# Kernel optimization log

Hardware: AMD Instinct MI355X
Metric: run time of the kernel (lower is better)

Reference implementation:

```python
import jax, jax.numpy as jnp
import numpy as np

N_PATCHES = 14
HIDDEN_D = 768
N_HEADS = 12
D_HEAD = HIDDEN_D // N_HEADS
OUT_D = 1000
IMG = 224
C = 3
PS = IMG // N_PATCHES  # 16
SEQ = N_PATCHES * N_PATCHES + 1  # 197
INPUT_D = C * PS * PS  # 768
EPS = 1e-5


def positional_embeddings(s, d):
    i = jnp.arange(s, dtype=jnp.float32)[:, None]
    j = jnp.arange(d, dtype=jnp.float32)[None, :]
    even = jnp.sin(i / jnp.power(10000.0, j / d))
    odd = jnp.cos(i / jnp.power(10000.0, (j - 1.0) / d))
    return jnp.where(jnp.arange(d)[None, :] % 2 == 0, even, odd)


def layernorm_2d(x, g, b):
    # torch nn.LayerNorm((S, D)): normalize over last two dims jointly, biased var
    mu = jnp.mean(x, axis=(-2, -1), keepdims=True)
    var = jnp.var(x, axis=(-2, -1), keepdims=True)
    return (x - mu) * jax.lax.rsqrt(var + EPS) * g + b


def setup_inputs() -> dict:
    key = jax.random.key(0)
    ks = jax.random.split(key, 16)
    s = 0.02
    return {
        "images": jax.random.normal(ks[0], (64, C, IMG, IMG), jnp.float32),
        "W_map": jax.random.normal(ks[1], (INPUT_D, HIDDEN_D), jnp.float32) * s,
        "b_map": jnp.zeros((HIDDEN_D,), jnp.float32),
        "cls_tok": jax.random.uniform(ks[2], (1, HIDDEN_D), jnp.float32),
        "ln1_g": jnp.ones((SEQ, HIDDEN_D), jnp.float32),
        "ln1_b": jnp.zeros((SEQ, HIDDEN_D), jnp.float32),
        "Wq": jax.random.normal(ks[3], (N_HEADS, D_HEAD, D_HEAD), jnp.float32) * s,
        "bq": jnp.zeros((N_HEADS, D_HEAD), jnp.float32),
        "Wk": jax.random.normal(ks[4], (N_HEADS, D_HEAD, D_HEAD), jnp.float32) * s,
        "bk": jnp.zeros((N_HEADS, D_HEAD), jnp.float32),
        "Wv": jax.random.normal(ks[5], (N_HEADS, D_HEAD, D_HEAD), jnp.float32) * s,
        "bv": jnp.zeros((N_HEADS, D_HEAD), jnp.float32),
        "ln2_g": jnp.ones((SEQ, HIDDEN_D), jnp.float32),
        "ln2_b": jnp.zeros((SEQ, HIDDEN_D), jnp.float32),
        "W_enc": jax.random.normal(ks[6], (HIDDEN_D, HIDDEN_D), jnp.float32) * s,
        "b_enc": jnp.zeros((HIDDEN_D,), jnp.float32),
        "W_out": jax.random.normal(ks[7], (HIDDEN_D, OUT_D), jnp.float32) * s,
        "b_out": jnp.zeros((OUT_D,), jnp.float32),
    }


def reference(images, W_map, b_map, cls_tok, ln1_g, ln1_b, Wq, bq, Wk, bk, Wv, bv,
              ln2_g, ln2_b, W_enc, b_enc, W_out, b_out):
    n = images.shape[0]
    # patchify: [N,C,H,W] -> [N, np*np, C*ps*ps], patch flattened in (C,ph,pw) order
    p = images.reshape(n, C, N_PATCHES, PS, N_PATCHES, PS)
    patches = p.transpose(0, 2, 4, 1, 3, 5).reshape(n, N_PATCHES * N_PATCHES, INPUT_D)

    tokens = patches @ W_map + b_map  # [N, np^2, D]
    cls = jnp.broadcast_to(cls_tok[None], (n, 1, HIDDEN_D))
    tokens = jnp.concatenate([cls, tokens], axis=1)  # [N, S, D]
    tokens = tokens + positional_embeddings(SEQ, HIDDEN_D)[None]

    # MSA on ln1(tokens), vectorized over batch and heads
    x = layernorm_2d(tokens, ln1_g, ln1_b)
    xh = x.reshape(n, SEQ, N_HEADS, D_HEAD)  # split hidden into heads
    q = jnp.einsum('bshd,hde->bshe', xh, Wq) + bq[None, None]
    k = jnp.einsum('bshd,hde->bshe', xh, Wk) + bk[None, None]
    v = jnp.einsum('bshd,hde->bshe', xh, Wv) + bv[None, None]
    scores = jnp.einsum('bshe,bthe->bhst', q, k) / np.sqrt(D_HEAD).astype(np.float32)
    attn = jax.nn.softmax(scores, axis=-1)  # [B,H,S,S]
    msa = jnp.einsum('bhst,bthe->bshe', attn, v).reshape(n, SEQ, HIDDEN_D)

    out = tokens + msa
    out = out + jax.nn.relu(layernorm_2d(out, ln2_g, ln2_b) @ W_enc + b_enc)
    cls_out = out[:, 0]  # [N, D]
    return jax.nn.softmax(cls_out @ W_out + b_out, axis=-1)
```

## Files before the change

kernel.cpp:

```cpp
#include <hip/hip_runtime.h>
#include <math.h>

#define SEQL 197
#define HD 768
#define NH 12
#define DHD 64
#define BATCH 64
#define OUTD 1000

typedef unsigned short ushort_t;
typedef __attribute__((ext_vector_type(8))) short bf16x8;
typedef __attribute__((ext_vector_type(4))) float f32x4;

static __device__ __forceinline__ unsigned short f2bf(float f) {
    union { float f; unsigned u; } v; v.f = f;
    unsigned r = v.u + 0x7fff + ((v.u >> 16) & 1);
    return (unsigned short)(r >> 16);
}

static __device__ __forceinline__ void gload16(const ushort_t* g, ushort_t* l) {
    __builtin_amdgcn_global_load_lds(
        (const __attribute__((address_space(1))) unsigned int*)g,
        (__attribute__((address_space(3))) unsigned int*)l, 16, 0, 0);
}

__global__ void k_init(const float* __restrict__ cls_tok, float* __restrict__ pos,
                       float* __restrict__ tok, float* __restrict__ stats) {
    int i = blockIdx.x * 256 + threadIdx.x;
    if (i < SEQL * HD) {
        int s = i / HD, d = i % HD;
        float f = (float)(d & ~1);
        float r = powf(10000.0f, -f / (float)HD);
        float a = (float)s * r;
        pos[i] = (d & 1) ? cosf(a) : sinf(a);
    } else {
        int j = i - SEQL * HD;
        if (j < BATCH * HD) {
            int b = j / HD, e = j % HD;
            float v = cls_tok[e] + ((e & 1) ? 1.0f : 0.0f);
            tok[(b * SEQL) * HD + e] = v;
            float sv = v, qv = v * v;
#pragma unroll
            for (int off = 32; off > 0; off >>= 1) {
                sv += __shfl_down(sv, off);
                qv += __shfl_down(qv, off);
            }
            if ((threadIdx.x & 63) == 0) {
                atomicAdd(&stats[2 * b], sv);
                atomicAdd(&stats[2 * b + 1], qv);
            }
        }
    }
}

__global__ void k_cvtAll(const float* __restrict__ W_map, const float* __restrict__ W_enc,
                         const float* __restrict__ Wq, const float* __restrict__ Wk,
                         const float* __restrict__ Wv,
                         ushort_t* __restrict__ WmT, ushort_t* __restrict__ WeT,
                         ushort_t* __restrict__ wt, float* __restrict__ stats) {
    int idx = blockIdx.x * 256 + threadIdx.x;
    if (blockIdx.x == 0 && threadIdx.x < 256) stats[threadIdx.x] = 0.f;
    if (idx < 2 * 147456) {
        const float* W = (idx < 147456) ? W_map : W_enc;
        ushort_t* WT   = (idx < 147456) ? WmT : WeT;
        int i = (idx < 147456) ? idx : idx - 147456;
        int k = i / 192, nq = i % 192;
        float4 w = *(const float4*)&W[k * 768 + nq * 4];
        WT[(nq * 4 + 0) * 768 + k] = f2bf(w.x);
        WT[(nq * 4 + 1) * 768 + k] = f2bf(w.y);
        WT[(nq * 4 + 2) * 768 + k] = f2bf(w.z);
        WT[(nq * 4 + 3) * 768 + k] = f2bf(w.w);
    } else {
        int i = idx - 2 * 147456;
        if (i < 36864) {
            int dq = i & 15;
            int e  = (i >> 4) & 63;
            int h  = (i >> 10) % 12;
            int pj = i / 12288;
            const float* W = (pj == 0) ? Wq : (pj == 1) ? Wk : Wv;
            ushort4 o;
            o.x = f2bf(W[(h * 64 + dq * 4 + 0) * 64 + e]);
            o.y = f2bf(W[(h * 64 + dq * 4 + 1) * 64 + e]);
            o.z = f2bf(W[(h * 64 + dq * 4 + 2) * 64 + e]);
            o.w = f2bf(W[(h * 64 + dq * 4 + 3) * 64 + e]);
            *(ushort4*)&wt[(size_t)((pj * 12 + h) * 64 + e) * 64 + dq * 4] = o;
        }
    }
}

__global__ void k_prep_patches(const float* __restrict__ img, ushort_t* __restrict__ Ae) {
    int idx = blockIdx.x * 256 + threadIdx.x;
    int m = idx / 192, kq = idx % 192;
    int k0 = kq * 4;
    int c = k0 >> 8, rem = k0 & 255, ir = rem >> 4, jc = rem & 15;
    int b = m / 196, pi = m % 196;
    int pr = pi / 14, pc = pi % 14;
    float4 v = *(const float4*)&img[((b * 3 + c) * 224 + pr * 16 + ir) * 224 + pc * 16 + jc];
    ushort4 o;
    o.x = f2bf(v.x); o.y = f2bf(v.y); o.z = f2bf(v.z); o.w = f2bf(v.w);
    *(ushort4*)&Ae[m * 768 + k0] = o;
}

template <int MODE>
__launch_bounds__(256)
__global__ void k_gemm_bf16(const ushort_t* __restrict__ A, const ushort_t* __restrict__ Bt,
                            const float* __restrict__ bias, const float* __restrict__ pos,
                            float* __restrict__ out, int Mtot, float* __restrict__ stats) {
    __shared__ ushort_t As[128 * 64];
    __shared__ ushort_t Bs[128 * 64];
    __shared__ float redS[4][4];
    const int m0 = blockIdx.x * 128;
    const int n0 = blockIdx.y * 128;
    const int tid = threadIdx.x;
    const int lane = tid & 63, wave = tid >> 6;
    const int wm = wave >> 1, wn = wave & 1;

    f32x4 acc[4][4];
#pragma unroll
    for (int i = 0; i < 4; ++i)
#pragma unroll
        for (int j = 0; j < 4; ++j)
#pragma unroll
            for (int r = 0; r < 4; ++r) acc[i][j][r] = 0.f;

    for (int kt = 0; kt < 12; ++kt) {
        const int k0 = kt * 64;
#pragma unroll
        for (int t = 0; t < 4; ++t) {
            int c = (wave << 2) | t;
            int o = c * 1024 + lane * 16;
            int row = o >> 7;
            int inner = o & 127;
            int col = (inner ^ ((row & 7) << 4)) >> 1;
            gload16(&A[(size_t)(m0 + row) * 768 + k0 + col], &As[c * 512]);
            gload16(&Bt[(size_t)(n0 + row) * 768 + k0 + col], &Bs[c * 512]);
        }
        __syncthreads();
#pragma unroll
        for (int ks = 0; ks < 2; ++ks) {
            const int cbyte = ks * 64 + (lane >> 4) * 16;
            bf16x8 af[4], bf[4];
#pragma unroll
            for (int mi = 0; mi < 4; ++mi) {
                int row = wm * 64 + mi * 16 + (lane & 15);
                af[mi] = *(const bf16x8*)((const char*)As + row * 128 + (cbyte ^ ((row & 7) << 4)));
            }
#pragma unroll
            for (int ni = 0; ni < 4; ++ni) {
                int n = wn * 64 + ni * 16 + (lane & 15);
                bf[ni] = *(const bf16x8*)((const char*)Bs + n * 128 + (cbyte ^ ((n & 7) << 4)));
            }
#pragma unroll
            for (int mi = 0; mi < 4; ++mi)
#pragma unroll
                for (int ni = 0; ni < 4; ++ni)
                    acc[mi][ni] = __builtin_amdgcn_mfma_f32_16x16x32_bf16(af[mi], bf[ni], acc[mi][ni], 0, 0, 0);
        }
        __syncthreads();
    }

    const int colb = n0 + wn * 64 + (lane & 15);
    const int rowb = m0 + wm * 64 + (lane >> 4) * 4;
    float s_lo = 0.f, q_lo = 0.f, s_hi = 0.f, q_hi = 0.f;
    const int bA = m0 / 196;
    const int mSplit = (bA + 1) * 196;
#pragma unroll
    for (int ni = 0; ni < 4; ++ni) {
        const int n = colb + ni * 16;
        const float bn = bias[n];
#pragma unroll
        for (int mi = 0; mi < 4; ++mi) {
#pragma unroll
            for (int r = 0; r < 4; ++r) {
                int m = rowb + mi * 16 + r;
                if (MODE == 0) {
                    int b = m / 196, s = 1 + m % 196;
                    float oval = acc[mi][ni][r] + bn + pos[s * HD + n];
                    out[((b * SEQL) + s) * HD + n] = oval;
                    if (m < mSplit) { s_lo += oval; q_lo += oval * oval; }
                    else            { s_hi += oval; q_hi += oval * oval; }
                } else {
                    if (m < Mtot) {
                        float* p = &out[(size_t)m * HD + n];
                        *p = *p + fmaxf(acc[mi][ni][r] + bn, 0.f);
                    }
                }
            }
        }
    }
    if (MODE == 0) {
#pragma unroll
        for (int off = 32; off > 0; off >>= 1) {
            s_lo += __shfl_down(s_lo, off);
            q_lo += __shfl_down(q_lo, off);
            s_hi += __shfl_down(s_hi, off);
            q_hi += __shfl_down(q_hi, off);
        }
        if (lane == 0) {
            redS[wave][0] = s_lo; redS[wave][1] = q_lo;
            redS[wave][2] = s_hi; redS[wave][3] = q_hi;
        }
        __syncthreads();
        if (tid == 0) {
            float a0 = 0.f, a1 = 0.f, a2 = 0.f, a3 = 0.f;
#pragma unroll
            for (int i = 0; i < 4; ++i) {
                a0 += redS[i][0]; a1 += redS[i][1];
                a2 += redS[i][2]; a3 += redS[i][3];
            }
            atomicAdd(&stats[2 * bA], a0);
            atomicAdd(&stats[2 * bA + 1], a1);
            int bB = bA + 1;
            if (bB < BATCH) {
                atomicAdd(&stats[2 * bB], a2);
                atomicAdd(&stats[2 * bB + 1], a3);
            }
        }
    }
}

__launch_bounds__(512, 2)
__global__ void k_qkvattn(const float* __restrict__ tok, float* __restrict__ stats,
                          const float* __restrict__ g1, const float* __restrict__ b1,
                          const ushort_t* __restrict__ wt,
                          const float* __restrict__ bq, const float* __restrict__ bk,
                          const float* __restrict__ bv, float* __restrict__ out) {
    const int h = blockIdx.x, b = blockIdx.y;
    __shared__ __attribute__((aligned(16))) ushort_t sm[51712];
    __shared__ float rS[8], rS2[8];
    const int tid = threadIdx.x;
    const int wave = tid >> 6, lane = tid & 63;
    const int l16 = lane & 15, l4 = lane >> 4;
    const int r0 = wave * 32;
    const float inv_n = 1.0f / (float)(SEQL * HD);
    const float S1_ = stats[b * 2], S2_ = stats[b * 2 + 1];
    const float mu = S1_ * inv_n;
    const float rsg = rsqrtf(S2_ * inv_n - mu * mu + 1e-5f);

    {
        const int row = tid >> 1, hw = tid & 1;
        if (row < SEQL) {
            const float* tp = &tok[((size_t)b * SEQL + row) * HD + h * 64 + hw * 32];
            const float* gp = &g1[(size_t)row * HD + h * 64 + hw * 32];
            const float* bp = &b1[(size_t)row * HD + h * 64 + hw * 32];
#pragma unroll
            for (int g = 0; g < 4; ++g) {
                float4 t0 = *(const float4*)&tp[g * 8];
                float4 t1 = *(const float4*)&tp[g * 8 + 4];
                float4 ga = *(const float4*)&gp[g * 8];
                float4 gb = *(const float4*)&gp[g * 8 + 4];
                float4 ba = *(const float4*)&bp[g * 8];
                float4 bb = *(const float4*)&bp[g * 8 + 4];
                bf16x8 o;
                o[0] = (short)f2bf((t0.x - mu) * rsg * ga.x + ba.x);
                o[1] = (short)f2bf((t0.y - mu) * rsg * ga.y + ba.y);
                o[2] = (short)f2bf((t0.z - mu) * rsg * ga.z + ba.z);
                o[3] = (short)f2bf((t0.w - mu) * rsg * ga.w + ba.w);
                o[4] = (short)f2bf((t1.x - mu) * rsg * gb.x + bb.x);
                o[5] = (short)f2bf((t1.y - mu) * rsg * gb.y + bb.y);
                o[6] = (short)f2bf((t1.z - mu) * rsg * gb.z + bb.z);
                o[7] = (short)f2bf((t1.w - mu) * rsg * gb.w + bb.w);
                int pc = (hw * 32 + g * 8) ^ ((row & 7) << 3);
                *(bf16x8*)&sm[row * 64 + pc] = o;
            }
        } else {
            bf16x8 z;
#pragma unroll
            for (int j = 0; j < 8; ++j) z[j] = 0;
#pragma unroll
            for (int g = 0; g < 4; ++g) {
                int pc = (hw * 32 + g * 8) ^ ((row & 7) << 3);
                *(bf16x8*)&sm[row * 64 + pc] = z;
            }
        }
    }

    bf16x8 af[2][2];
#pragma unroll
    for (int mi = 0; mi < 2; ++mi)
#pragma unroll
        for (int kk = 0; kk < 2; ++kk) {
            int row = r0 + mi * 16 + l16;
            af[mi][kk] = *(const bf16x8*)&sm[row * 64 + ((kk * 32 + l4 * 8) ^ ((row & 7) << 3))];
        }

    ushort_t* myS = &sm[wave * 2048];

#define PROJ_ACC(PJ, ACC)                                                                      \
    {                                                                                          \
        _Pragma("unroll") for (int ni = 0; ni < 4; ++ni) {                                     \
            const ushort_t* wr = &wt[(size_t)(((PJ) * 12 + h) * 64 + ni * 16 + l16) * 64];     \
            bf16x8 w0 = *(const bf16x8*)&wr[l4 * 8];                                           \
            bf16x8 w1 = *(const bf16x8*)&wr[32 + l4 * 8];                                      \
            _Pragma("unroll") for (int mi = 0; mi < 2; ++mi) {                                 \
                ACC[mi][ni] = __builtin_amdgcn_mfma_f32_16x16x32_bf16(af[mi][0], w0, ACC[mi][ni], 0, 0, 0); \
                ACC[mi][ni] = __builtin_amdgcn_mfma_f32_16x16x32_bf16(af[mi][1], w1, ACC[mi][ni], 0, 0, 0); \
            }                                                                                  \
        }                                                                                      \
    }

    f32x4 acc[2][4];
#define ZERO_ACC                                                                               \
    _Pragma("unroll") for (int mi = 0; mi < 2; ++mi)                                           \
        _Pragma("unroll") for (int ni = 0; ni < 4; ++ni) {                                     \
            acc[mi][ni][0] = 0.f; acc[mi][ni][1] = 0.f; acc[mi][ni][2] = 0.f; acc[mi][ni][3] = 0.f; }

    ZERO_ACC;
    PROJ_ACC(0, acc);
#pragma unroll
    for (int ni = 0; ni < 4; ++ni) {
        float bn = bq[h * 64 + ni * 16 + l16];
#pragma unroll
        for (int mi = 0; mi < 2; ++mi)
#pragma unroll
            for (int r = 0; r < 4; ++r) {
                int rl = mi * 16 + l4 * 4 + r;
                myS[rl * 64 + ((ni * 16 + l16) ^ ((rl & 7) << 3))] = f2bf(acc[mi][ni][r] + bn);
            }
    }
    bf16x8 qa[2][2];
#pragma unroll
    for (int mi = 0; mi < 2; ++mi)
#pragma unroll
        for (int kk = 0; kk < 2; ++kk) {
            int rl = mi * 16 + l16;
            qa[mi][kk] = *(const bf16x8*)&myS[rl * 64 + ((kk * 32 + l4 * 8) ^ ((rl & 7) << 3))];
        }

    ZERO_ACC;
    PROJ_ACC(1, acc);
#pragma unroll
    for (int ni = 0; ni < 4; ++ni) {
        float bn = bk[h * 64 + ni * 16 + l16];
#pragma unroll
        for (int mi = 0; mi < 2; ++mi)
#pragma unroll
            for (int r = 0; r < 4; ++r) {
                int t = r0 + mi * 16 + l4 * 4 + r;
                sm[16384 + t * 72 + ni * 16 + l16] = f2bf(acc[mi][ni][r] + bn);
            }
    }

    ZERO_ACC;
    PROJ_ACC(2, acc);
#pragma unroll
    for (int ni = 0; ni < 4; ++ni) {
        float bn = bv[h * 64 + ni * 16 + l16];
#pragma unroll
        for (int mi = 0; mi < 2; ++mi)
#pragma unroll
            for (int r = 0; r < 4; ++r) {
                int t = r0 + mi * 16 + l4 * 4 + r;
                sm[34816 + (ni * 16 + l16) * 264 + t] = f2bf(acc[mi][ni][r] + bn);
            }
    }

    __syncthreads();

    f32x4 sa[2][16];
#pragma unroll
    for (int ni = 0; ni < 16; ++ni) {
        int t = ni * 16 + l16;
        bf16x8 k0 = *(const bf16x8*)&sm[16384 + t * 72 + l4 * 8];
        bf16x8 k1 = *(const bf16x8*)&sm[16384 + t * 72 + 32 + l4 * 8];
#pragma unroll
        for (int mi = 0; mi < 2; ++mi) {
            f32x4 z;
            z[0] = 0.f; z[1] = 0.f; z[2] = 0.f; z[3] = 0.f;
            z = __builtin_amdgcn_mfma_f32_16x16x32_bf16(qa[mi][0], k0, z, 0, 0, 0);
            sa[mi][ni] = __builtin_amdgcn_mfma_f32_16x16x32_bf16(qa[mi][1], k1, z, 0, 0, 0);
        }
    }

    float l_s[2][4];
#pragma unroll
    for (int mi = 0; mi < 2; ++mi)
#pragma unroll
        for (int r = 0; r < 4; ++r) {
            float rsum = 0.f;
#pragma unroll
            for (int ni = 0; ni < 16; ++ni) {
                float p = (ni * 16 + l16 < SEQL) ? __expf(sa[mi][ni][r] * 0.125f) : 0.f;
                sa[mi][ni][r] = p;
                rsum += p;
            }
            rsum += __shfl_xor(rsum, 1);
            rsum += __shfl_xor(rsum, 2);
            rsum += __shfl_xor(rsum, 4);
            rsum += __shfl_xor(rsum, 8);
            l_s[mi][r] = rsum;
        }

    f32x4 oacc[2][4];
#pragma unroll
    for (int mi = 0; mi < 2; ++mi)
#pragma unroll
        for (int ne = 0; ne < 4; ++ne) {
            oacc[mi][ne][0] = 0.f; oacc[mi][ne][1] = 0.f;
            oacc[mi][ne][2] = 0.f; oacc[mi][ne][3] = 0.f;
        }

    for (int c = 0; c < 4; ++c) {
#pragma unroll
        for (int j = 0; j < 4; ++j)
#pragma unroll
            for (int mi = 0; mi < 2; ++mi)
#pragma unroll
                for (int r = 0; r < 4; ++r) {
                    int rl = mi * 16 + l4 * 4 + r;
                    myS[rl * 64 + ((j * 16 + l16) ^ ((rl & 7) << 3))] = f2bf(sa[mi][c * 4 + j][r]);
                }
        bf16x8 pa[2][2];
#pragma unroll
        for (int mi = 0; mi < 2; ++mi)
#pragma unroll
            for (int kk = 0; kk < 2; ++kk) {
                int rl = mi * 16 + l16;
                pa[mi][kk] = *(const bf16x8*)&myS[rl * 64 + ((kk * 32 + l4 * 8) ^ ((rl & 7) << 3))];
            }
#pragma unroll
        for (int ne = 0; ne < 4; ++ne) {
            int e = ne * 16 + l16;
            bf16x8 v0 = *(const bf16x8*)&sm[34816 + e * 264 + c * 64 + l4 * 8];
            bf16x8 v1 = *(const bf16x8*)&sm[34816 + e * 264 + c * 64 + 32 + l4 * 8];
#pragma unroll
            for (int mi = 0; mi < 2; ++mi) {
                oacc[mi][ne] = __builtin_amdgcn_mfma_f32_16x16x32_bf16(pa[mi][0], v0, oacc[mi][ne], 0, 0, 0);
                oacc[mi][ne] = __builtin_amdgcn_mfma_f32_16x16x32_bf16(pa[mi][1], v1, oacc[mi][ne], 0, 0, 0);
            }
        }
    }

    __syncthreads();
    float* Osm = (float*)&sm[16384] + wave * 2176;
#pragma unroll
    for (int mi = 0; mi < 2; ++mi)
#pragma unroll
        for (int r = 0; r < 4; ++r) {
            float inv = 1.0f / l_s[mi][r];
            int rl = mi * 16 + l4 * 4 + r;
#pragma unroll
            for (int ne = 0; ne < 4; ++ne)
                Osm[rl * 68 + ne * 16 + l16] = oacc[mi][ne][r] * inv;
        }
    float psum = 0.f, psq = 0.f;
#pragma unroll
    for (int it = 0; it < 8; ++it) {
        int rl = it * 4 + l4;
        int row = r0 + rl;
        if (row < SEQL) {
            size_t off = ((size_t)b * SEQL + row) * HD + h * 64 + l16 * 4;
            float4 ov = *(float4*)&Osm[rl * 68 + l16 * 4];
            float4 tv = *(const float4*)&tok[off];
            float4 o;
            o.x = ov.x + tv.x; o.y = ov.y + tv.y;
            o.z = ov.z + tv.z; o.w = ov.w + tv.w;
            *(float4*)&out[off] = o;
            psum += o.x + o.y + o.z + o.w;
            psq  += o.x * o.x + o.y * o.y + o.z * o.z + o.w * o.w;
        }
    }
#pragma unroll
    for (int off = 32; off > 0; off >>= 1) {
        psum += __shfl_down(psum, off);
        psq += __shfl_down(psq, off);
    }
    if (lane == 0) { rS[wave] = psum; rS2[wave] = psq; }
    __syncthreads();
    if (tid == 0) {
        float S = 0.f, S2 = 0.f;
#pragma unroll
        for (int i = 0; i < 8; ++i) { S += rS[i]; S2 += rS2[i]; }
        atomicAdd(&stats[128 + 2 * b], S);
        atomicAdd(&stats[129 + 2 * b], S2);
    }
#undef PROJ_ACC
#undef ZERO_ACC
}

__global__ void k_ln2apply(const float* __restrict__ outb, const float* __restrict__ stats,
                           const float* __restrict__ g2, const float* __restrict__ b2,
                           ushort_t* __restrict__ x) {
    int i = blockIdx.x * 256 + threadIdx.x;
    if (i >= BATCH * SEQL * HD / 4) return;
    int e4 = i * 4;
    int m = e4 / HD, kk = e4 % HD;
    int b = m / SEQL, s = m % SEQL;
    const float inv_n = 1.0f / (float)(SEQL * HD);
    float S = stats[128 + 2 * b], S2 = stats[129 + 2 * b];
    float mu = S * inv_n;
    float rsg = rsqrtf(S2 * inv_n - mu * mu + 1e-5f);
    float4 t = *(const float4*)&outb[e4];
    float4 g = *(const float4*)&g2[s * HD + kk];
    float4 bb = *(const float4*)&b2[s * HD + kk];
    ushort4 o;
    o.x = f2bf((t.x - mu) * rsg * g.x + bb.x);
    o.y = f2bf((t.y - mu) * rsg * g.y + bb.y);
    o.z = f2bf((t.z - mu) * rsg * g.z + bb.z);
    o.w = f2bf((t.w - mu) * rsg * g.w + bb.w);
    *(ushort4*)&x[e4] = o;
}

__launch_bounds__(256)
__global__ void k_head(const float* __restrict__ out, const float* __restrict__ Wo,
                       const float* __restrict__ bo, float* __restrict__ dout) {
    const int b = blockIdx.x, tid = threadIdx.x;
    __shared__ float cls[768];
    __shared__ float red[256];
    for (int i = tid; i < 192; i += 256)
        *(float4*)&cls[i * 4] = *(const float4*)&out[(b * SEQL) * HD + i * 4];
    __syncthreads();

    const int o0 = tid * 4;
    const bool ok = (o0 < OUTD);
    float4 acc = {0.f, 0.f, 0.f, 0.f};
    if (ok) {
        acc = *(const float4*)&bo[o0];
        for (int e = 0; e < 768; ++e) {
            float c = cls[e];
            float4 w = *(const float4*)&Wo[e * OUTD + o0];
            acc.x += c * w.x;
            acc.y += c * w.y;
            acc.z += c * w.z;
            acc.w += c * w.w;
        }
    }
    float mx = ok ? fmaxf(fmaxf(acc.x, acc.y), fmaxf(acc.z, acc.w)) : -INFINITY;
    red[tid] = mx;
    __syncthreads();
    for (int s = 128; s > 0; s >>= 1) {
        if (tid < s) red[tid] = fmaxf(red[tid], red[tid + s]);
        __syncthreads();
    }
    float M = red[0];
    __syncthreads();
    float4 p = {0.f, 0.f, 0.f, 0.f};
    float ls = 0.f;
    if (ok) {
        p.x = expf(acc.x - M);
        p.y = expf(acc.y - M);
        p.z = expf(acc.z - M);
        p.w = expf(acc.w - M);
        ls = p.x + p.y + p.z + p.w;
    }
    red[tid] = ls;
    __syncthreads();
    for (int s = 128; s > 0; s >>= 1) {
        if (tid < s) red[tid] += red[tid + s];
        __syncthreads();
    }
    float inv = 1.0f / red[0];
    if (ok) {
        p.x *= inv; p.y *= inv; p.z *= inv; p.w *= inv;
        *(float4*)&dout[b * OUTD + o0] = p;
    }
}

extern "C" void kernel_launch(void* const* d_in, const int* in_sizes, int n_in,
                              void* d_out, int out_size, void* d_ws, size_t ws_size,
                              hipStream_t stream) {
    const float* images  = (const float*)d_in[0];
    const float* W_map   = (const float*)d_in[1];
    const float* b_map   = (const float*)d_in[2];
    const float* cls_tok = (const float*)d_in[3];
    const float* ln1_g   = (const float*)d_in[4];
    const float* ln1_b   = (const float*)d_in[5];
    const float* Wq      = (const float*)d_in[6];
    const float* bq      = (const float*)d_in[7];
    const float* Wk      = (const float*)d_in[8];
    const float* bk      = (const float*)d_in[9];
    const float* Wv      = (const float*)d_in[10];
    const float* bv      = (const float*)d_in[11];
    const float* ln2_g   = (const float*)d_in[12];
    const float* ln2_b   = (const float*)d_in[13];
    const float* W_enc   = (const float*)d_in[14];
    const float* b_enc   = (const float*)d_in[15];
    const float* W_out   = (const float*)d_in[16];
    const float* b_out   = (const float*)d_in[17];

    float* ws = (float*)d_ws;
    const size_t BIG = (size_t)BATCH * SEQL * HD;

    float* pos   = ws;
    float* tok   = ws + 151552;
    float* outb  = tok + BIG;
    float* stats = outb + BIG;
    ushort_t* wtq = (ushort_t*)(stats + 256);
    ushort_t* Ae  = wtq + 147456;
    ushort_t* WmT = Ae + (size_t)12672 * 768;
    ushort_t* WeT = WmT + (size_t)768 * 768;
    ushort_t* Ae2 = Ae;

    k_cvtAll<<<1296, 256, 0, stream>>>(W_map, W_enc, Wq, Wk, Wv, WmT, WeT, wtq, stats);
    k_init<<<783, 256, 0, stream>>>(cls_tok, pos, tok, stats);
    k_prep_patches<<<9408, 256, 0, stream>>>(images, Ae);
    k_gemm_bf16<0><<<dim3(98, 6), 256, 0, stream>>>(Ae, WmT, b_map, pos, tok, 12544, stats);
    k_qkvattn<<<dim3(12, 64), 512, 0, stream>>>(tok, stats, ln1_g, ln1_b, wtq, bq, bk, bv, outb);
    k_ln2apply<<<9456, 256, 0, stream>>>(outb, stats, ln2_g, ln2_b, Ae2);
    k_gemm_bf16<1><<<dim3(99, 6), 256, 0, stream>>>(Ae2, WeT, b_enc, pos, outb, 12608, stats);
    k_head<<<64, 256, 0, stream>>>(outb, W_out, b_out, (float*)d_out);
}
```

Before: 261.7 us.

## Shrink attention kernel LDS and registers to fit four blocks per CU

The fused QKV+attention kernel's shared memory drops from about 101KB to 64KB. LN1 output is loaded straight into registers instead of staged through LDS, Q/K/P reuse one swizzled buffer, and V is stored in a swizzled transposed layout. The exp and row-sum are folded into the QK^T loop and the probabilities kept packed as bf16, which removes the fp32 score array and cuts register use. Launch bounds rise to 4 blocks per CU to hide latency, with an extra barrier and a risk of spills under the tighter register budget.

```diff
diff --git a/kernel.cpp b/kernel.cpp
--- a/kernel.cpp
+++ b/kernel.cpp
@@ -219,14 +219,14 @@
     }
 }
 
-__launch_bounds__(512, 2)
+__launch_bounds__(512, 4)
 __global__ void k_qkvattn(const float* __restrict__ tok, float* __restrict__ stats,
                           const float* __restrict__ g1, const float* __restrict__ b1,
                           const ushort_t* __restrict__ wt,
                           const float* __restrict__ bq, const float* __restrict__ bk,
                           const float* __restrict__ bv, float* __restrict__ out) {
     const int h = blockIdx.x, b = blockIdx.y;
-    __shared__ __attribute__((aligned(16))) ushort_t sm[51712];
+    __shared__ __attribute__((aligned(16))) ushort_t sm[32768];
     __shared__ float rS[8], rS2[8];
     const int tid = threadIdx.x;
     const int wave = tid >> 6, lane = tid & 63;
@@ -236,55 +236,37 @@
     const float S1_ = stats[b * 2], S2_ = stats[b * 2 + 1];
     const float mu = S1_ * inv_n;
     const float rsg = rsqrtf(S2_ * inv_n - mu * mu + 1e-5f);
-
-    {
-        const int row = tid >> 1, hw = tid & 1;
-        if (row < SEQL) {
-            const float* tp = &tok[((size_t)b * SEQL + row) * HD + h * 64 + hw * 32];
-            const float* gp = &g1[(size_t)row * HD + h * 64 + hw * 32];
-            const float* bp = &b1[(size_t)row * HD + h * 64 + hw * 32];
-#pragma unroll
-            for (int g = 0; g < 4; ++g) {
-                float4 t0 = *(const float4*)&tp[g * 8];
-                float4 t1 = *(const float4*)&tp[g * 8 + 4];
-                float4 ga = *(const float4*)&gp[g * 8];
-                float4 gb = *(const float4*)&gp[g * 8 + 4];
-                float4 ba = *(const float4*)&bp[g * 8];
-                float4 bb = *(const float4*)&bp[g * 8 + 4];
-                bf16x8 o;
-                o[0] = (short)f2bf((t0.x - mu) * rsg * ga.x + ba.x);
-                o[1] = (short)f2bf((t0.y - mu) * rsg * ga.y + ba.y);
-                o[2] = (short)f2bf((t0.z - mu) * rsg * ga.z + ba.z);
-                o[3] = (short)f2bf((t0.w - mu) * rsg * ga.w + ba.w);
-                o[4] = (short)f2bf((t1.x - mu) * rsg * gb.x + bb.x);
-                o[5] = (short)f2bf((t1.y - mu) * rsg * gb.y + bb.y);
-                o[6] = (short)f2bf((t1.z - mu) * rsg * gb.z + bb.z);
-                o[7] = (short)f2bf((t1.w - mu) * rsg * gb.w + bb.w);
-                int pc = (hw * 32 + g * 8) ^ ((row & 7) << 3);
-                *(bf16x8*)&sm[row * 64 + pc] = o;
-            }
-        } else {
-            bf16x8 z;
-#pragma unroll
-            for (int j = 0; j < 8; ++j) z[j] = 0;
-#pragma unroll
-            for (int g = 0; g < 4; ++g) {
-                int pc = (hw * 32 + g * 8) ^ ((row & 7) << 3);
-                *(bf16x8*)&sm[row * 64 + pc] = z;
-            }
-        }
+    ushort_t* A16 = sm;
+    ushort_t* B16 = sm + 16384;
+
+#define LDX(dst, s, d0)                                                                  \
+    {                                                                                    \
+        if ((s) < SEQL) {                                                                \
+            const float* tp = &tok[((size_t)b * SEQL + (s)) * HD + h * 64 + (d0)];       \
+            const float* gp = &g1[(size_t)(s) * HD + h * 64 + (d0)];                     \
+            const float* bp = &b1[(size_t)(s) * HD + h * 64 + (d0)];                     \
+            float4 t0 = *(const float4*)&tp[0], t1 = *(const float4*)&tp[4];             \
+            float4 ga = *(const float4*)&gp[0], gb = *(const float4*)&gp[4];             \
+            float4 ba = *(const float4*)&bp[0], bb = *(const float4*)&bp[4];             \
+            dst[0] = (short)f2bf((t0.x - mu) * rsg * ga.x + ba.x);                       \
+            dst[1] = (short)f2bf((t0.y - mu) * rsg * ga.y + ba.y);                       \
+            dst[2] = (short)f2bf((t0.z - mu) * rsg * ga.z + ba.z);                       \
+            dst[3] = (short)f2bf((t0.w - mu) * rsg * ga.w + ba.w);                       \
+            dst[4] = (short)f2bf((t1.x - mu) * rsg * gb.x + bb.x);                       \
+            dst[5] = (short)f2bf((t1.y - mu) * rsg * gb.y + bb.y);                       \
+            dst[6] = (short)f2bf((t1.z - mu) * rsg * gb.z + bb.z);                       \
+            dst[7] = (short)f2bf((t1.w - mu) * rsg * gb.w + bb.w);                       \
+        } else {                                                                         \
+            _Pragma("unroll") for (int _j = 0; _j < 8; ++_j) dst[_j] = 0;                \
+        }                                                                                \
     }
 
     bf16x8 af[2][2];
 #pragma unroll
     for (int mi = 0; mi < 2; ++mi)
 #pragma unroll
-        for (int kk = 0; kk < 2; ++kk) {
-            int row = r0 + mi * 16 + l16;
-            af[mi][kk] = *(const bf16x8*)&sm[row * 64 + ((kk * 32 + l4 * 8) ^ ((row & 7) << 3))];
-        }
-
-    ushort_t* myS = &sm[wave * 2048];
+        for (int kk = 0; kk < 2; ++kk)
+            LDX(af[mi][kk], r0 + mi * 16 + l16, kk * 32 + l4 * 8);
 
 #define PROJ_ACC(PJ, ACC)                                                                      \
     {                                                                                          \
@@ -314,8 +296,8 @@
         for (int mi = 0; mi < 2; ++mi)
 #pragma unroll
             for (int r = 0; r < 4; ++r) {
-                int rl = mi * 16 + l4 * 4 + r;
-                myS[rl * 64 + ((ni * 16 + l16) ^ ((rl & 7) << 3))] = f2bf(acc[mi][ni][r] + bn);
+                int row = r0 + mi * 16 + l4 * 4 + r;
+                A16[row * 64 + ((ni * 16 + l16) ^ ((row & 7) << 3))] = f2bf(acc[mi][ni][r] + bn);
             }
     }
     bf16x8 qa[2][2];
@@ -323,8 +305,8 @@
     for (int mi = 0; mi < 2; ++mi)
 #pragma unroll
         for (int kk = 0; kk < 2; ++kk) {
-            int rl = mi * 16 + l16;
-            qa[mi][kk] = *(const bf16x8*)&myS[rl * 64 + ((kk * 32 + l4 * 8) ^ ((rl & 7) << 3))];
+            int row = r0 + mi * 16 + l16;
+            qa[mi][kk] = *(const bf16x8*)&A16[row * 64 + ((kk * 32 + l4 * 8) ^ ((row & 7) << 3))];
         }
 
     ZERO_ACC;
@@ -337,7 +319,7 @@
 #pragma unroll
             for (int r = 0; r < 4; ++r) {
                 int t = r0 + mi * 16 + l4 * 4 + r;
-                sm[16384 + t * 72 + ni * 16 + l16] = f2bf(acc[mi][ni][r] + bn);
+                A16[t * 64 + ((ni * 16 + l16) ^ ((t & 7) << 3))] = f2bf(acc[mi][ni][r] + bn);
             }
     }
 
@@ -347,49 +329,63 @@
     for (int ni = 0; ni < 4; ++ni) {
         float bn = bv[h * 64 + ni * 16 + l16];
 #pragma unroll
-        for (int mi = 0; mi < 2; ++mi)
-#pragma unroll
-            for (int r = 0; r < 4; ++r) {
-                int t = r0 + mi * 16 + l4 * 4 + r;
-                sm[34816 + (ni * 16 + l16) * 264 + t] = f2bf(acc[mi][ni][r] + bn);
-            }
-    }
-
-    __syncthreads();
-
-    f32x4 sa[2][16];
+        for (int mi = 0; mi < 2; ++mi) {
+            int t4 = r0 + mi * 16 + l4 * 4;
+            int e = ni * 16 + l16;
+            ushort4 pkt;
+            pkt.x = f2bf(acc[mi][ni][0] + bn);
+            pkt.y = f2bf(acc[mi][ni][1] + bn);
+            pkt.z = f2bf(acc[mi][ni][2] + bn);
+            pkt.w = f2bf(acc[mi][ni][3] + bn);
+            *(ushort4*)&B16[e * 256 + (t4 ^ ((e & 7) << 3))] = pkt;
+        }
+    }
+
+    __syncthreads();
+
+    unsigned pk[2][16][2];
+    float rsum[2][4];
+#pragma unroll
+    for (int mi = 0; mi < 2; ++mi)
+#pragma unroll
+        for (int r = 0; r < 4; ++r) rsum[mi][r] = 0.f;
+
 #pragma unroll
     for (int ni = 0; ni < 16; ++ni) {
-        int t = ni * 16 + l16;
-        bf16x8 k0 = *(const bf16x8*)&sm[16384 + t * 72 + l4 * 8];
-        bf16x8 k1 = *(const bf16x8*)&sm[16384 + t * 72 + 32 + l4 * 8];
+        const int t = ni * 16 + l16;
+        bf16x8 k0 = *(const bf16x8*)&A16[t * 64 + ((l4 * 8) ^ ((t & 7) << 3))];
+        bf16x8 k1 = *(const bf16x8*)&A16[t * 64 + ((32 + l4 * 8) ^ ((t & 7) << 3))];
+        const bool valid = (t < SEQL);
 #pragma unroll
         for (int mi = 0; mi < 2; ++mi) {
             f32x4 z;
             z[0] = 0.f; z[1] = 0.f; z[2] = 0.f; z[3] = 0.f;
             z = __builtin_amdgcn_mfma_f32_16x16x32_bf16(qa[mi][0], k0, z, 0, 0, 0);
-            sa[mi][ni] = __builtin_amdgcn_mfma_f32_16x16x32_bf16(qa[mi][1], k1, z, 0, 0, 0);
-        }
-    }
-
+            z = __builtin_amdgcn_mfma_f32_16x16x32_bf16(qa[mi][1], k1, z, 0, 0, 0);
+            float p0 = valid ? __expf(z[0] * 0.125f) : 0.f;
+            float p1 = valid ? __expf(z[1] * 0.125f) : 0.f;
+            float p2 = valid ? __expf(z[2] * 0.125f) : 0.f;
+            float p3 = valid ? __expf(z[3] * 0.125f) : 0.f;
+            rsum[mi][0] += p0; rsum[mi][1] += p1;
+            rsum[mi][2] += p2; rsum[mi][3] += p3;
+            pk[mi][ni][0] = (unsigned)f2bf(p0) | ((unsigned)f2bf(p1) << 16);
+            pk[mi][ni][1] = (unsigned)f2bf(p2) | ((unsigned)f2bf(p3) << 16);
+        }
+    }
     float l_s[2][4];
 #pragma unroll
     for (int mi = 0; mi < 2; ++mi)
 #pragma unroll
         for (int r = 0; r < 4; ++r) {
-            float rsum = 0.f;
-#pragma unroll
-            for (int ni = 0; ni < 16; ++ni) {
-                float p = (ni * 16 + l16 < SEQL) ? __expf(sa[mi][ni][r] * 0.125f) : 0.f;
-                sa[mi][ni][r] = p;
-                rsum += p;
-            }
-            rsum += __shfl_xor(rsum, 1);
-            rsum += __shfl_xor(rsum, 2);
-            rsum += __shfl_xor(rsum, 4);
-            rsum += __shfl_xor(rsum, 8);
-            l_s[mi][r] = rsum;
-        }
+            float rs_ = rsum[mi][r];
+            rs_ += __shfl_xor(rs_, 1);
+            rs_ += __shfl_xor(rs_, 2);
+            rs_ += __shfl_xor(rs_, 4);
+            rs_ += __shfl_xor(rs_, 8);
+            l_s[mi][r] = rs_;
+        }
+
+    __syncthreads();
 
     f32x4 oacc[2][4];
 #pragma unroll
@@ -400,6 +396,7 @@
             oacc[mi][ne][2] = 0.f; oacc[mi][ne][3] = 0.f;
         }
 
+#pragma unroll
     for (int c = 0; c < 4; ++c) {
 #pragma unroll
         for (int j = 0; j < 4; ++j)
@@ -407,22 +404,23 @@
             for (int mi = 0; mi < 2; ++mi)
 #pragma unroll
                 for (int r = 0; r < 4; ++r) {
-                    int rl = mi * 16 + l4 * 4 + r;
-                    myS[rl * 64 + ((j * 16 + l16) ^ ((rl & 7) << 3))] = f2bf(sa[mi][c * 4 + j][r]);
+                    int row = r0 + mi * 16 + l4 * 4 + r;
+                    ushort_t pv = (ushort_t)(pk[mi][c * 4 + j][r >> 1] >> ((r & 1) * 16));
+                    A16[row * 64 + ((j * 16 + l16) ^ ((row & 7) << 3))] = pv;
                 }
         bf16x8 pa[2][2];
 #pragma unroll
         for (int mi = 0; mi < 2; ++mi)
 #pragma unroll
             for (int kk = 0; kk < 2; ++kk) {
-                int rl = mi * 16 + l16;
-                pa[mi][kk] = *(const bf16x8*)&myS[rl * 64 + ((kk * 32 + l4 * 8) ^ ((rl & 7) << 3))];
+                int row = r0 + mi * 16 + l16;
+                pa[mi][kk] = *(const bf16x8*)&A16[row * 64 + ((kk * 32 + l4 * 8) ^ ((row & 7) << 3))];
             }
 #pragma unroll
         for (int ne = 0; ne < 4; ++ne) {
             int e = ne * 16 + l16;
-            bf16x8 v0 = *(const bf16x8*)&sm[34816 + e * 264 + c * 64 + l4 * 8];
-            bf16x8 v1 = *(const bf16x8*)&sm[34816 + e * 264 + c * 64 + 32 + l4 * 8];
+            bf16x8 v0 = *(const bf16x8*)&B16[e * 256 + ((c * 64 + l4 * 8) ^ ((e & 7) << 3))];
+            bf16x8 v1 = *(const bf16x8*)&B16[e * 256 + ((c * 64 + 32 + l4 * 8) ^ ((e & 7) << 3))];
 #pragma unroll
             for (int mi = 0; mi < 2; ++mi) {
                 oacc[mi][ne] = __builtin_amdgcn_mfma_f32_16x16x32_bf16(pa[mi][0], v0, oacc[mi][ne], 0, 0, 0);
@@ -432,7 +430,7 @@
     }
 
     __syncthreads();
-    float* Osm = (float*)&sm[16384] + wave * 2176;
+    float* Osm = (float*)sm + wave * 2048;
 #pragma unroll
     for (int mi = 0; mi < 2; ++mi)
 #pragma unroll
@@ -441,7 +439,7 @@
             int rl = mi * 16 + l4 * 4 + r;
 #pragma unroll
             for (int ne = 0; ne < 4; ++ne)
-                Osm[rl * 68 + ne * 16 + l16] = oacc[mi][ne][r] * inv;
+                Osm[rl * 64 + ((ne * 16 + l16) ^ ((rl & 3) << 4))] = oacc[mi][ne][r] * inv;
         }
     float psum = 0.f, psq = 0.f;
 #pragma unroll
@@ -450,7 +448,7 @@
         int row = r0 + rl;
         if (row < SEQL) {
             size_t off = ((size_t)b * SEQL + row) * HD + h * 64 + l16 * 4;
-            float4 ov = *(float4*)&Osm[rl * 68 + l16 * 4];
+            float4 ov = *(float4*)&Osm[rl * 64 + ((l16 * 4) ^ ((rl & 3) << 4))];
             float4 tv = *(const float4*)&tok[off];
             float4 o;
             o.x = ov.x + tv.x; o.y = ov.y + tv.y;
@@ -476,6 +474,7 @@
     }
 #undef PROJ_ACC
 #undef ZERO_ACC
+#undef LDX
 }
 
 __global__ void k_ln2apply(const float* __restrict__ outb, const float* __restrict__ stats,
```

New measurement: 299.6 us. 14.5% more time.

## Alias Q, P and K buffers in one LDS region to shrink shared memory

Applied to the files above, without the earlier changes.

Reuses a single padded row-major LDS region (stride 72) for the normalized input, Q staging, K and the per-wave P tiles, which shrinks the kernel's shared memory allocation. The V transpose store is packed into 4-element vector writes. An extra block barrier is added before P overwrites K rows so the aliasing stays correct. The aim is lower LDS footprint, which may allow more blocks per CU, and fewer LDS store instructions, at the cost of one more synchronization.

```diff
diff --git a/kernel.cpp b/kernel.cpp
--- a/kernel.cpp
+++ b/kernel.cpp
@@ -226,7 +226,7 @@
                           const float* __restrict__ bq, const float* __restrict__ bk,
                           const float* __restrict__ bv, float* __restrict__ out) {
     const int h = blockIdx.x, b = blockIdx.y;
-    __shared__ __attribute__((aligned(16))) ushort_t sm[51712];
+    __shared__ __attribute__((aligned(16))) ushort_t sm[35328];
     __shared__ float rS[8], rS2[8];
     const int tid = threadIdx.x;
     const int wave = tid >> 6, lane = tid & 63;
@@ -236,6 +236,8 @@
     const float S1_ = stats[b * 2], S2_ = stats[b * 2 + 1];
     const float mu = S1_ * inv_n;
     const float rsg = rsqrtf(S2_ * inv_n - mu * mu + 1e-5f);
+    ushort_t* Kr = sm;
+    ushort_t* Vr = sm + 18432;
 
     {
         const int row = tid >> 1, hw = tid & 1;
@@ -261,7 +263,7 @@
                 o[6] = (short)f2bf((t1.z - mu) * rsg * gb.z + bb.z);
                 o[7] = (short)f2bf((t1.w - mu) * rsg * gb.w + bb.w);
                 int pc = (hw * 32 + g * 8) ^ ((row & 7) << 3);
-                *(bf16x8*)&sm[row * 64 + pc] = o;
+                *(bf16x8*)&Kr[row * 72 + pc] = o;
             }
         } else {
             bf16x8 z;
@@ -270,7 +272,7 @@
 #pragma unroll
             for (int g = 0; g < 4; ++g) {
                 int pc = (hw * 32 + g * 8) ^ ((row & 7) << 3);
-                *(bf16x8*)&sm[row * 64 + pc] = z;
+                *(bf16x8*)&Kr[row * 72 + pc] = z;
             }
         }
     }
@@ -281,10 +283,8 @@
 #pragma unroll
         for (int kk = 0; kk < 2; ++kk) {
             int row = r0 + mi * 16 + l16;
-            af[mi][kk] = *(const bf16x8*)&sm[row * 64 + ((kk * 32 + l4 * 8) ^ ((row & 7) << 3))];
-        }
-
-    ushort_t* myS = &sm[wave * 2048];
+            af[mi][kk] = *(const bf16x8*)&Kr[row * 72 + ((kk * 32 + l4 * 8) ^ ((row & 7) << 3))];
+        }
 
 #define PROJ_ACC(PJ, ACC)                                                                      \
     {                                                                                          \
@@ -314,8 +314,8 @@
         for (int mi = 0; mi < 2; ++mi)
 #pragma unroll
             for (int r = 0; r < 4; ++r) {
-                int rl = mi * 16 + l4 * 4 + r;
-                myS[rl * 64 + ((ni * 16 + l16) ^ ((rl & 7) << 3))] = f2bf(acc[mi][ni][r] + bn);
+                int row = r0 + mi * 16 + l4 * 4 + r;
+                Kr[row * 72 + ((ni * 16 + l16) ^ ((row & 7) << 3))] = f2bf(acc[mi][ni][r] + bn);
             }
     }
     bf16x8 qa[2][2];
@@ -323,8 +323,8 @@
     for (int mi = 0; mi < 2; ++mi)
 #pragma unroll
         for (int kk = 0; kk < 2; ++kk) {
-            int rl = mi * 16 + l16;
-            qa[mi][kk] = *(const bf16x8*)&myS[rl * 64 + ((kk * 32 + l4 * 8) ^ ((rl & 7) << 3))];
+            int row = r0 + mi * 16 + l16;
+            qa[mi][kk] = *(const bf16x8*)&Kr[row * 72 + ((kk * 32 + l4 * 8) ^ ((row & 7) << 3))];
         }
 
     ZERO_ACC;
@@ -337,7 +337,7 @@
 #pragma unroll
             for (int r = 0; r < 4; ++r) {
                 int t = r0 + mi * 16 + l4 * 4 + r;
-                sm[16384 + t * 72 + ni * 16 + l16] = f2bf(acc[mi][ni][r] + bn);
+                Kr[t * 72 + ni * 16 + l16] = f2bf(acc[mi][ni][r] + bn);
             }
     }
 
@@ -347,12 +347,16 @@
     for (int ni = 0; ni < 4; ++ni) {
         float bn = bv[h * 64 + ni * 16 + l16];
 #pragma unroll
-        for (int mi = 0; mi < 2; ++mi)
-#pragma unroll
-            for (int r = 0; r < 4; ++r) {
-                int t = r0 + mi * 16 + l4 * 4 + r;
-                sm[34816 + (ni * 16 + l16) * 264 + t] = f2bf(acc[mi][ni][r] + bn);
-            }
+        for (int mi = 0; mi < 2; ++mi) {
+            int t4 = r0 + mi * 16 + l4 * 4;
+            int e = ni * 16 + l16;
+            ushort4 pkt;
+            pkt.x = f2bf(acc[mi][ni][0] + bn);
+            pkt.y = f2bf(acc[mi][ni][1] + bn);
+            pkt.z = f2bf(acc[mi][ni][2] + bn);
+            pkt.w = f2bf(acc[mi][ni][3] + bn);
+            *(ushort4*)&Vr[e * 264 + t4] = pkt;
+        }
     }
 
     __syncthreads();
@@ -361,8 +365,8 @@
 #pragma unroll
     for (int ni = 0; ni < 16; ++ni) {
         int t = ni * 16 + l16;
-        bf16x8 k0 = *(const bf16x8*)&sm[16384 + t * 72 + l4 * 8];
-        bf16x8 k1 = *(const bf16x8*)&sm[16384 + t * 72 + 32 + l4 * 8];
+        bf16x8 k0 = *(const bf16x8*)&Kr[t * 72 + l4 * 8];
+        bf16x8 k1 = *(const bf16x8*)&Kr[t * 72 + 32 + l4 * 8];
 #pragma unroll
         for (int mi = 0; mi < 2; ++mi) {
             f32x4 z;
@@ -391,6 +395,8 @@
             l_s[mi][r] = rsum;
         }
 
+    __syncthreads();
+
     f32x4 oacc[2][4];
 #pragma unroll
     for (int mi = 0; mi < 2; ++mi)
@@ -407,22 +413,22 @@
             for (int mi = 0; mi < 2; ++mi)
 #pragma unroll
                 for (int r = 0; r < 4; ++r) {
-                    int rl = mi * 16 + l4 * 4 + r;
-                    myS[rl * 64 + ((j * 16 + l16) ^ ((rl & 7) << 3))] = f2bf(sa[mi][c * 4 + j][r]);
+                    int row = r0 + mi * 16 + l4 * 4 + r;
+                    Kr[row * 72 + ((j * 16 + l16) ^ ((row & 7) << 3))] = f2bf(sa[mi][c * 4 + j][r]);
                 }
         bf16x8 pa[2][2];
 #pragma unroll
         for (int mi = 0; mi < 2; ++mi)
 #pragma unroll
             for (int kk = 0; kk < 2; ++kk) {
-                int rl = mi * 16 + l16;
-                pa[mi][kk] = *(const bf16x8*)&myS[rl * 64 + ((kk * 32 + l4 * 8) ^ ((rl & 7) << 3))];
+                int row = r0 + mi * 16 + l16;
+                pa[mi][kk] = *(const bf16x8*)&Kr[row * 72 + ((kk * 32 + l4 * 8) ^ ((row & 7) << 3))];
             }
 #pragma unroll
         for (int ne = 0; ne < 4; ++ne) {
             int e = ne * 16 + l16;
-            bf16x8 v0 = *(const bf16x8*)&sm[34816 + e * 264 + c * 64 + l4 * 8];
-            bf16x8 v1 = *(const bf16x8*)&sm[34816 + e * 264 + c * 64 + 32 + l4 * 8];
+            bf16x8 v0 = *(const bf16x8*)&Vr[e * 264 + c * 64 + l4 * 8];
+            bf16x8 v1 = *(const bf16x8*)&Vr[e * 264 + c * 64 + 32 + l4 * 8];
 #pragma unroll
             for (int mi = 0; mi < 2; ++mi) {
                 oacc[mi][ne] = __builtin_amdgcn_mfma_f32_16x16x32_bf16(pa[mi][0], v0, oacc[mi][ne], 0, 0, 0);
@@ -432,7 +438,7 @@
     }
 
     __syncthreads();
-    float* Osm = (float*)&sm[16384] + wave * 2176;
+    float* Osm = (float*)sm + wave * 2176;
 #pragma unroll
     for (int mi = 0; mi < 2; ++mi)
 #pragma unroll
```

Measured after the change: 262.2 us. No clear change (+0.2%).
